# Kernel tuning notes

Hardware: AMD Instinct MI355X
Metric: run time of the kernel (lower is better)

The kernel has to match this reference:

```python
import jax, jax.numpy as jnp
import numpy as np

B, N, DM, H, C, DC = 4, 1024, 512, 8, 3, 16  # batch, nodes, node_dim, heads, manifold components, per-component dim
DK = DM // H


def setup_inputs() -> dict:
    key = jax.random.key(0)
    ks = jax.random.split(key, 8)

    def lin_w(k):
        return jax.random.normal(k, (DM, DM), jnp.float32) / np.sqrt(DM).astype(np.float32)

    return {
        "h": jax.random.normal(ks[0], (B, N, DM), jnp.float32),
        "x": jax.random.normal(ks[1], (B, N, C * DC), jnp.float32),
        "Wq": lin_w(ks[2]), "bq": jnp.zeros((DM,), jnp.float32),
        "Wk": lin_w(ks[3]), "bk": jnp.zeros((DM,), jnp.float32),
        "Wv": lin_w(ks[4]), "bv": jnp.zeros((DM,), jnp.float32),
        "Wo": lin_w(ks[5]), "bo": jnp.zeros((DM,), jnp.float32),
        "alpha": jnp.ones((H, C), jnp.float32),
        "log_sigma": jnp.zeros((H, C), jnp.float32),
    }


def reference(h, x, Wq, bq, Wk, bk, Wv, bv, Wo, bo, alpha, log_sigma):
    b, n, dm = h.shape
    hh, cc = alpha.shape
    dk = dm // hh
    scale = 1.0 / np.sqrt(dk).astype(np.float32)

    def to_heads(t, W, bias):
        return (t @ W.T + bias).reshape(b, n, hh, dk).transpose(0, 2, 1, 3)  # (B,H,N,dk)

    Q = to_heads(h, Wq, bq)
    K = to_heads(h, Wk, bk)
    V = to_heads(h, Wv, bv)

    attn = jnp.einsum('bhid,bhjd->bhij', Q, K) * scale  # (B,H,N,N)

    # Geodesic kernel: per-component Euclidean distances on the product manifold.
    xs = x.reshape(b, n, cc, -1)                      # (B,N,C,dc)
    sq = jnp.sum(xs * xs, axis=-1)                    # (B,N,C)
    inner = jnp.einsum('bicd,bjcd->bijc', xs, xs)     # (B,N,N,C)
    d_sq = jnp.maximum(sq[:, :, None, :] + sq[:, None, :, :] - 2.0 * inner, 0.0)  # (B,N,N,C)

    sigma = jnp.clip(jnp.exp(log_sigma), 1e-4)        # (H,C)
    # exp(-d_c^2 / (2 sigma_{h,c}^2)) -> (B,H,N,N,C), then weight by alpha and sum over c
    e = jnp.exp(-d_sq[:, None] / (2.0 * (sigma ** 2)[None, :, None, None, :])).astype(attn.dtype)
    attn = attn + jnp.einsum('hc,bhijc->bhij', alpha, e)

    p = jax.nn.softmax(attn, axis=-1)
    out = jnp.einsum('bhij,bhjd->bhid', p, V)         # (B,H,N,dk)
    out = out.transpose(0, 2, 1, 3).reshape(b, n, dm)
    return out @ Wo.T + bo
```

## Files before the change

kernel.cpp:

```cpp
#include <hip/hip_runtime.h>
#include <math.h>

typedef __bf16 bf16;
typedef __attribute__((ext_vector_type(8))) __bf16 bf16x8;
typedef __attribute__((ext_vector_type(4))) float f32x4;

#define LOG2E 1.44269504088896f
#define SCALE 0.125f

__device__ inline f32x4 mfma16(bf16x8 a, bf16x8 b, f32x4 c) {
    return __builtin_amdgcn_mfma_f32_16x16x32_bf16(a, b, c, 0, 0, 0);
}
__device__ inline bf16x8 cvt8(float4 v0, float4 v1) {
    bf16x8 o;
    o[0] = (bf16)v0.x; o[1] = (bf16)v0.y; o[2] = (bf16)v0.z; o[3] = (bf16)v0.w;
    o[4] = (bf16)v1.x; o[5] = (bf16)v1.y; o[6] = (bf16)v1.z; o[7] = (bf16)v1.w;
    return o;
}
__device__ inline float fastexp2(float x) {
    float r;
    asm("v_exp_f32 %0, %1" : "=v"(r) : "v"(x));
    return r;
}

__global__ __launch_bounds__(256) void gemm_qkv_kernel(
        const float* __restrict__ A, const float* __restrict__ Wq,
        const float* __restrict__ Wk, const float* __restrict__ Wv,
        const float* __restrict__ bq, const float* __restrict__ bk,
        const float* __restrict__ bv,
        bf16* __restrict__ Qb, bf16* __restrict__ Kb, bf16* __restrict__ Vt) {
    __shared__ bf16 smem[64 * 72 + 128 * 72];
    bf16 (*Asm)[72] = (bf16(*)[72])smem;
    bf16 (*Bsm)[72] = (bf16(*)[72])(smem + 64 * 72);
    int t = threadIdx.x, w = t >> 6, lane = t & 63, g = lane >> 4, lo = lane & 15;
    int rowbase = blockIdx.x * 64, colbase = blockIdx.y * 128;
    int proj = colbase >> 9, wcol = colbase & 511;
    const float* Wsrc = (proj == 0) ? Wq : (proj == 1 ? Wk : Wv);
    const float* bsrc = (proj == 0) ? bq : (proj == 1 ? bk : bv);
    int wr = (w >> 1) * 32, wc = (w & 1) * 64;
    f32x4 acc[2][4] = {};
    int arow = t >> 2, acol = (t & 3) * 16;
    int brow = t >> 1, bcol = (t & 1) * 32;
    for (int kb = 0; kb < 512; kb += 64) {
        __syncthreads();
        {
            const float4* as = (const float4*)&A[(size_t)(rowbase + arow) * 512 + kb + acol];
            *(bf16x8*)&Asm[arow][acol]     = cvt8(as[0], as[1]);
            *(bf16x8*)&Asm[arow][acol + 8] = cvt8(as[2], as[3]);
            const float4* bs = (const float4*)&Wsrc[(size_t)(wcol + brow) * 512 + kb + bcol];
            *(bf16x8*)&Bsm[brow][bcol]      = cvt8(bs[0], bs[1]);
            *(bf16x8*)&Bsm[brow][bcol + 8]  = cvt8(bs[2], bs[3]);
            *(bf16x8*)&Bsm[brow][bcol + 16] = cvt8(bs[4], bs[5]);
            *(bf16x8*)&Bsm[brow][bcol + 24] = cvt8(bs[6], bs[7]);
        }
        __syncthreads();
        for (int kk = 0; kk < 64; kk += 32) {
            bf16x8 af[2], bfr[4];
            for (int m = 0; m < 2; m++) af[m]  = *(const bf16x8*)&Asm[wr + 16 * m + lo][kk + 8 * g];
            for (int n = 0; n < 4; n++) bfr[n] = *(const bf16x8*)&Bsm[wc + 16 * n + lo][kk + 8 * g];
            for (int m = 0; m < 2; m++)
                for (int n = 0; n < 4; n++)
                    acc[m][n] = mfma16(af[m], bfr[n], acc[m][n]);
        }
    }
    __syncthreads();
    bf16 (*Cl)[132] = (bf16(*)[132])smem;
    for (int n = 0; n < 4; n++) {
        float bv = bsrc[wcol + wc + 16 * n + lo];
        for (int m = 0; m < 2; m++)
            for (int r = 0; r < 4; r++)
                Cl[wr + 16 * m + 4 * g + r][wc + 16 * n + lo] = (bf16)(acc[m][n][r] + bv);
    }
    __syncthreads();
    int h0 = (colbase >> 6) & 7;
    int bidx = rowbase >> 10, i0g = rowbase & 1023;
    if (proj < 2) {
        int row = t >> 2, q4 = t & 3;
        int head = h0 + (q4 >> 1), d0 = (q4 & 1) * 32;
        bf16* dst = (proj == 0 ? Qb : Kb) +
                    ((size_t)(bidx * 8 + head) * 1024 + i0g + row) * 64 + d0;
        for (int ch = 0; ch < 4; ch++)
            *(bf16x8*)&dst[ch * 8] = *(const bf16x8*)&Cl[row][(q4 >> 1) * 64 + d0 + ch * 8];
    } else {
        int dcol = t >> 1, ihalf = t & 1;
        int head = h0 + (dcol >> 6), d = dcol & 63;
        bf16* dst = Vt + ((size_t)(bidx * 8 + head) * 64 + d) * 1024 + i0g + ihalf * 32;
        for (int ch = 0; ch < 4; ch++) {
            bf16x8 v;
            for (int q = 0; q < 8; q++) v[q] = Cl[ihalf * 32 + ch * 8 + q][dcol];
            *(bf16x8*)&dst[ch * 8] = v;
        }
    }
}

__global__ __launch_bounds__(256) void attn_kernel(
        const bf16* __restrict__ Qb, const bf16* __restrict__ Kb,
        const bf16* __restrict__ Vt, const float* __restrict__ x,
        const float* __restrict__ alpha, const float* __restrict__ log_sigma,
        float* __restrict__ o_part, float* __restrict__ l_part) {
    __shared__ bf16 Klds[64][72];
    __shared__ bf16 VTlds[64][72];
    __shared__ bf16 Xlds[64][80];
    __shared__ bf16 Plds[4][16][72];

    int t = threadIdx.x;
    int w = t >> 6, lane = t & 63, g = lane >> 4, lo = lane & 15;
    int zz = blockIdx.z;
    int b = zz >> 1, split = zz & 1;
    int hh = blockIdx.y;
    int i0 = blockIdx.x * 64 + w * 16;

    float c1 = SCALE * LOG2E;
    float k2[3], alf[3];
    for (int c = 0; c < 3; c++) {
        float sg = fmaxf(expf(log_sigma[hh * 3 + c]), 1e-4f);
        k2[c] = LOG2E / (sg * sg);
        alf[c] = alpha[hh * 3 + c] * LOG2E;
    }

    const bf16* Qbase = Qb + ((size_t)(b * 8 + hh) * 1024 + i0) * 64;
    bf16x8 qa[2];
    qa[0] = *(const bf16x8*)&Qbase[lo * 64 + 8 * g];
    qa[1] = *(const bf16x8*)&Qbase[lo * 64 + 32 + 8 * g];

    bf16x8 xqa[3];
    for (int c = 0; c < 3; c++) {
        bf16x8 v = {};
        if (g < 2) {
            const float4* xs = (const float4*)&x[((size_t)(b << 10) + i0 + lo) * 48 + c * 16 + 8 * g];
            v = cvt8(xs[0], xs[1]);
        } else if (g == 2) {
            const float* xr = &x[((size_t)(b << 10) + i0 + lo) * 48 + c * 16];
            float s = 0.0f;
            for (int k = 0; k < 16; k++) {
                float vv = (float)(bf16)xr[k];
                s += vv * vv;
            }
            s = -0.5f * s;
            bf16 sh = (bf16)s;
            v[0] = sh;
            v[1] = (bf16)(s - (float)sh);
            v[2] = (bf16)1.0f;
            v[3] = (bf16)1.0f;
        }
        xqa[c] = v;
    }

    bf16x8 ones;
    for (int e = 0; e < 8; e++) ones[e] = (bf16)1.0f;
    f32x4 o[4] = {};
    f32x4 lacc = {};

    for (int idx = t; idx < 64; idx += 256)
        *(uint4*)&Xlds[idx][72] = (uint4){0, 0, 0, 0};

    int sr = t >> 2, sc = (t & 3) * 16;
    int jb = split * 512;
    for (int j0 = jb; j0 < jb + 512; j0 += 64) {
        __syncthreads();
        const bf16* Kbase = Kb + ((size_t)(b * 8 + hh) * 1024 + j0) * 64;
        *(bf16x8*)&Klds[sr][sc]     = *(const bf16x8*)&Kbase[sr * 64 + sc];
        *(bf16x8*)&Klds[sr][sc + 8] = *(const bf16x8*)&Kbase[sr * 64 + sc + 8];
        const bf16* Vbase = Vt + ((size_t)(b * 8 + hh) * 64) * 1024 + j0;
        *(bf16x8*)&VTlds[sr][sc]     = *(const bf16x8*)&Vbase[sr * 1024 + sc];
        *(bf16x8*)&VTlds[sr][sc + 8] = *(const bf16x8*)&Vbase[sr * 1024 + sc + 8];
        if (t < 192) {
            int xr = t / 3, c = t - xr * 3;
            const float4* xs = (const float4*)&x[((size_t)(b << 10) + j0 + xr) * 48 + c * 16];
            bf16x8 d0 = cvt8(xs[0], xs[1]);
            bf16x8 d1 = cvt8(xs[2], xs[3]);
            *(bf16x8*)&Xlds[xr][c * 24]     = d0;
            *(bf16x8*)&Xlds[xr][c * 24 + 8] = d1;
            float s = 0.0f;
            for (int k = 0; k < 8; k++) {
                float a0 = (float)d0[k], a1 = (float)d1[k];
                s += a0 * a0 + a1 * a1;
            }
            s = -0.5f * s;
            bf16 sh = (bf16)s;
            bf16x8 cst = {};
            cst[0] = (bf16)1.0f;
            cst[1] = (bf16)1.0f;
            cst[2] = sh;
            cst[3] = (bf16)(s - (float)sh);
            *(bf16x8*)&Xlds[xr][c * 24 + 16] = cst;
        }
        __syncthreads();

        for (int tt = 0; tt < 4; tt++) {
            f32x4 acc = {};
            bf16x8 kb0 = *(const bf16x8*)&Klds[16 * tt + lo][8 * g];
            bf16x8 kb1 = *(const bf16x8*)&Klds[16 * tt + lo][32 + 8 * g];
            __builtin_amdgcn_s_setprio(1);
            acc = mfma16(qa[0], kb0, acc);
            acc = mfma16(qa[1], kb1, acc);
            f32x4 z0 = {}, z1 = {}, z2 = {};
            f32x4 e0 = mfma16(xqa[0], *(const bf16x8*)&Xlds[16 * tt + lo][8 * g], z0);
            f32x4 e1 = mfma16(xqa[1], *(const bf16x8*)&Xlds[16 * tt + lo][24 + 8 * g], z1);
            f32x4 e2 = mfma16(xqa[2], *(const bf16x8*)&Xlds[16 * tt + lo][48 + 8 * g], z2);
            __builtin_amdgcn_s_setprio(0);
            for (int r = 0; r < 4; r++) {
                float t0 = alf[0] * fastexp2(k2[0] * fminf(e0[r], 0.0f));
                t0 = fmaf(alf[1], fastexp2(k2[1] * fminf(e1[r], 0.0f)), t0);
                t0 = fmaf(alf[2], fastexp2(k2[2] * fminf(e2[r], 0.0f)), t0);
                float p = fastexp2(fmaf(acc[r], c1, t0));
                Plds[w][4 * g + r][16 * tt + lo] = (bf16)p;
            }
        }

        bf16x8 pa0 = *(const bf16x8*)&Plds[w][lo][8 * g];
        bf16x8 pa1 = *(const bf16x8*)&Plds[w][lo][32 + 8 * g];
        __builtin_amdgcn_s_setprio(1);
        lacc = mfma16(pa0, ones, lacc);
        lacc = mfma16(pa1, ones, lacc);
        for (int td = 0; td < 4; td++) {
            bf16x8 vb0 = *(const bf16x8*)&VTlds[16 * td + lo][8 * g];
            bf16x8 vb1 = *(const bf16x8*)&VTlds[16 * td + lo][32 + 8 * g];
            o[td] = mfma16(pa0, vb0, o[td]);
            o[td] = mfma16(pa1, vb1, o[td]);
        }
        __builtin_amdgcn_s_setprio(0);
    }

    for (int td = 0; td < 4; td++)
        for (int r = 0; r < 4; r++) {
            size_t rowg = (size_t)(b * 8 + hh) * 1024 + i0 + 4 * g + r;
            o_part[((size_t)split * 32768 + rowg) * 64 + 16 * td + lo] = o[td][r];
        }
    if (lo == 0)
        for (int r = 0; r < 4; r++) {
            size_t rowg = (size_t)(b * 8 + hh) * 1024 + i0 + 4 * g + r;
            l_part[(size_t)split * 32768 + rowg] = lacc[r];
        }
}

__global__ __launch_bounds__(256) void gemm_out_kernel(
        const float* __restrict__ o_part, const float* __restrict__ l_part,
        const float* __restrict__ Wo, const float* __restrict__ bo,
        float* __restrict__ out) {
    __shared__ bf16 Asm[64][72];
    __shared__ bf16 Bsm[64][72];
    int t = threadIdx.x, w = t >> 6, lane = t & 63, g = lane >> 4, lo = lane & 15;
    int rowbase = blockIdx.x * 64, colbase = blockIdx.y * 64;
    int wr = (w >> 1) * 32, wc = (w & 1) * 32;
    f32x4 acc[2][2] = {};
    int srow = t >> 2, scol = (t & 3) * 16;
    for (int kb = 0; kb < 512; kb += 64) {
        __syncthreads();
        {
            int hh = kb >> 6;
            int n = rowbase + srow;
            size_t rowg = (size_t)((n >> 10) * 8 + hh) * 1024 + (n & 1023);
            const float* p0 = &o_part[rowg * 64 + scol];
            const float* p1 = &o_part[((size_t)32768 + rowg) * 64 + scol];
            float inv = 1.0f / (l_part[rowg] + l_part[32768 + rowg]);
            float4 a0 = ((const float4*)p0)[0], a1 = ((const float4*)p0)[1];
            float4 a2 = ((const float4*)p0)[2], a3 = ((const float4*)p0)[3];
            float4 c0 = ((const float4*)p1)[0], c1 = ((const float4*)p1)[1];
            float4 c2 = ((const float4*)p1)[2], c3 = ((const float4*)p1)[3];
            bf16x8 r0, r1;
            r0[0] = (bf16)((a0.x + c0.x) * inv); r0[1] = (bf16)((a0.y + c0.y) * inv);
            r0[2] = (bf16)((a0.z + c0.z) * inv); r0[3] = (bf16)((a0.w + c0.w) * inv);
            r0[4] = (bf16)((a1.x + c1.x) * inv); r0[5] = (bf16)((a1.y + c1.y) * inv);
            r0[6] = (bf16)((a1.z + c1.z) * inv); r0[7] = (bf16)((a1.w + c1.w) * inv);
            r1[0] = (bf16)((a2.x + c2.x) * inv); r1[1] = (bf16)((a2.y + c2.y) * inv);
            r1[2] = (bf16)((a2.z + c2.z) * inv); r1[3] = (bf16)((a2.w + c2.w) * inv);
            r1[4] = (bf16)((a3.x + c3.x) * inv); r1[5] = (bf16)((a3.y + c3.y) * inv);
            r1[6] = (bf16)((a3.z + c3.z) * inv); r1[7] = (bf16)((a3.w + c3.w) * inv);
            *(bf16x8*)&Asm[srow][scol]     = r0;
            *(bf16x8*)&Asm[srow][scol + 8] = r1;
        }
        {
            const float4* bs = (const float4*)&Wo[(size_t)(colbase + srow) * 512 + kb + scol];
            *(bf16x8*)&Bsm[srow][scol]     = cvt8(bs[0], bs[1]);
            *(bf16x8*)&Bsm[srow][scol + 8] = cvt8(bs[2], bs[3]);
        }
        __syncthreads();
        for (int kk = 0; kk < 64; kk += 32) {
            bf16x8 af[2], bfr[2];
            for (int m = 0; m < 2; m++) af[m]  = *(const bf16x8*)&Asm[wr + 16 * m + lo][kk + 8 * g];
            for (int n = 0; n < 2; n++) bfr[n] = *(const bf16x8*)&Bsm[wc + 16 * n + lo][kk + 8 * g];
            for (int m = 0; m < 2; m++)
                for (int n = 0; n < 2; n++)
                    acc[m][n] = mfma16(af[m], bfr[n], acc[m][n]);
        }
    }
    for (int n = 0; n < 2; n++) {
        int mcol = colbase + wc + 16 * n + lo;
        float bv = bo[mcol];
        for (int m = 0; m < 2; m++)
            for (int r = 0; r < 4; r++)
                out[(size_t)(rowbase + wr + 16 * m + 4 * g + r) * 512 + mcol] =
                    acc[m][n][r] + bv;
    }
}

extern "C" void kernel_launch(void* const* d_in, const int* in_sizes, int n_in,
                              void* d_out, int out_size, void* d_ws, size_t ws_size,
                              hipStream_t stream) {
    const float* h  = (const float*)d_in[0];
    const float* x  = (const float*)d_in[1];
    const float* Wq = (const float*)d_in[2];
    const float* bq = (const float*)d_in[3];
    const float* Wk = (const float*)d_in[4];
    const float* bk = (const float*)d_in[5];
    const float* Wv = (const float*)d_in[6];
    const float* bv = (const float*)d_in[7];
    const float* Wo = (const float*)d_in[8];
    const float* bo = (const float*)d_in[9];
    const float* alpha     = (const float*)d_in[10];
    const float* log_sigma = (const float*)d_in[11];
    float* out = (float*)d_out;

    char* ws = (char*)d_ws;
    size_t off = 0;
    auto alloc = [&](size_t bytes) {
        char* p = ws + off;
        off += (bytes + 255) & ~(size_t)255;
        return p;
    };
    bf16*  Qb     = (bf16*)alloc((size_t)4 * 8 * 1024 * 64 * 2);
    bf16*  Kb     = (bf16*)alloc((size_t)4 * 8 * 1024 * 64 * 2);
    bf16*  Vt     = (bf16*)alloc((size_t)4 * 8 * 1024 * 64 * 2);
    float* o_part = (float*)alloc((size_t)2 * 32768 * 64 * 4);
    float* l_part = (float*)alloc((size_t)2 * 32768 * 4);

    gemm_qkv_kernel<<<dim3(64, 12), 256, 0, stream>>>(h, Wq, Wk, Wv, bq, bk, bv,
                                                      Qb, Kb, Vt);
    attn_kernel<<<dim3(16, 8, 8), 256, 0, stream>>>(
        Qb, Kb, Vt, x, alpha, log_sigma, o_part, l_part);
    gemm_out_kernel<<<dim3(64, 8), 256, 0, stream>>>(o_part, l_part, Wo, bo, out);
}
```

Baseline: 169.5 us.

## Prefetch next tile's global loads into registers across all three kernels

Each main loop in the QKV GEMM, the fused attention kernel and the output GEMM now issues the global loads for the next K-tile into registers right after the LDS barrier, before the MFMA work. The aim is to overlap global memory latency with compute instead of stalling at the top of each iteration. MFMA sections are wrapped in s_setprio, and the output normalisation uses a v_rcp_f32 reciprocal instead of a divide. This raises register pressure, which could lower occupancy.

Measured after the change: 172.6 us. No clear change (+1.8%).

```diff
diff --git a/kernel.cpp b/kernel.cpp
--- a/kernel.cpp
+++ b/kernel.cpp
@@ -20,6 +20,11 @@
 __device__ inline float fastexp2(float x) {
     float r;
     asm("v_exp_f32 %0, %1" : "=v"(r) : "v"(x));
+    return r;
+}
+__device__ inline float fastrcp(float x) {
+    float r;
+    asm("v_rcp_f32 %0, %1" : "=v"(r) : "v"(x));
     return r;
 }
 
@@ -41,19 +46,31 @@
     f32x4 acc[2][4] = {};
     int arow = t >> 2, acol = (t & 3) * 16;
     int brow = t >> 1, bcol = (t & 1) * 32;
+    const float* aptr = &A[(size_t)(rowbase + arow) * 512 + acol];
+    const float* bptr = &Wsrc[(size_t)(wcol + brow) * 512 + bcol];
+    float4 ar[4], br[8];
+    {
+        const float4* as = (const float4*)aptr;
+        ar[0] = as[0]; ar[1] = as[1]; ar[2] = as[2]; ar[3] = as[3];
+        const float4* bs = (const float4*)bptr;
+        for (int q = 0; q < 8; q++) br[q] = bs[q];
+    }
     for (int kb = 0; kb < 512; kb += 64) {
         __syncthreads();
-        {
-            const float4* as = (const float4*)&A[(size_t)(rowbase + arow) * 512 + kb + acol];
-            *(bf16x8*)&Asm[arow][acol]     = cvt8(as[0], as[1]);
-            *(bf16x8*)&Asm[arow][acol + 8] = cvt8(as[2], as[3]);
-            const float4* bs = (const float4*)&Wsrc[(size_t)(wcol + brow) * 512 + kb + bcol];
-            *(bf16x8*)&Bsm[brow][bcol]      = cvt8(bs[0], bs[1]);
-            *(bf16x8*)&Bsm[brow][bcol + 8]  = cvt8(bs[2], bs[3]);
-            *(bf16x8*)&Bsm[brow][bcol + 16] = cvt8(bs[4], bs[5]);
-            *(bf16x8*)&Bsm[brow][bcol + 24] = cvt8(bs[6], bs[7]);
-        }
-        __syncthreads();
+        *(bf16x8*)&Asm[arow][acol]     = cvt8(ar[0], ar[1]);
+        *(bf16x8*)&Asm[arow][acol + 8] = cvt8(ar[2], ar[3]);
+        *(bf16x8*)&Bsm[brow][bcol]      = cvt8(br[0], br[1]);
+        *(bf16x8*)&Bsm[brow][bcol + 8]  = cvt8(br[2], br[3]);
+        *(bf16x8*)&Bsm[brow][bcol + 16] = cvt8(br[4], br[5]);
+        *(bf16x8*)&Bsm[brow][bcol + 24] = cvt8(br[6], br[7]);
+        __syncthreads();
+        if (kb + 64 < 512) {
+            const float4* as = (const float4*)(aptr + kb + 64);
+            ar[0] = as[0]; ar[1] = as[1]; ar[2] = as[2]; ar[3] = as[3];
+            const float4* bs = (const float4*)(bptr + kb + 64);
+            for (int q = 0; q < 8; q++) br[q] = bs[q];
+        }
+        __builtin_amdgcn_s_setprio(1);
         for (int kk = 0; kk < 64; kk += 32) {
             bf16x8 af[2], bfr[4];
             for (int m = 0; m < 2; m++) af[m]  = *(const bf16x8*)&Asm[wr + 16 * m + lo][kk + 8 * g];
@@ -62,6 +79,7 @@
                 for (int n = 0; n < 4; n++)
                     acc[m][n] = mfma16(af[m], bfr[n], acc[m][n]);
         }
+        __builtin_amdgcn_s_setprio(0);
     }
     __syncthreads();
     bf16 (*Cl)[132] = (bf16(*)[132])smem;
@@ -155,22 +173,36 @@
         *(uint4*)&Xlds[idx][72] = (uint4){0, 0, 0, 0};
 
     int sr = t >> 2, sc = (t & 3) * 16;
+    int xr = t / 3, xc = t - xr * 3;
+    const bf16* Kbase0 = Kb + (size_t)(b * 8 + hh) * 1024 * 64;
+    const bf16* Vbase  = Vt + (size_t)(b * 8 + hh) * 64 * 1024;
     int jb = split * 512;
+
+    bf16x8 pk0, pk1, pv0, pv1;
+    float4 pxs[4];
+    {
+        const bf16* Kp = Kbase0 + (size_t)jb * 64;
+        pk0 = *(const bf16x8*)&Kp[sr * 64 + sc];
+        pk1 = *(const bf16x8*)&Kp[sr * 64 + sc + 8];
+        pv0 = *(const bf16x8*)&Vbase[sr * 1024 + jb + sc];
+        pv1 = *(const bf16x8*)&Vbase[sr * 1024 + jb + sc + 8];
+        if (t < 192) {
+            const float4* xs = (const float4*)&x[((size_t)(b << 10) + jb + xr) * 48 + xc * 16];
+            for (int q = 0; q < 4; q++) pxs[q] = xs[q];
+        }
+    }
+
     for (int j0 = jb; j0 < jb + 512; j0 += 64) {
         __syncthreads();
-        const bf16* Kbase = Kb + ((size_t)(b * 8 + hh) * 1024 + j0) * 64;
-        *(bf16x8*)&Klds[sr][sc]     = *(const bf16x8*)&Kbase[sr * 64 + sc];
-        *(bf16x8*)&Klds[sr][sc + 8] = *(const bf16x8*)&Kbase[sr * 64 + sc + 8];
-        const bf16* Vbase = Vt + ((size_t)(b * 8 + hh) * 64) * 1024 + j0;
-        *(bf16x8*)&VTlds[sr][sc]     = *(const bf16x8*)&Vbase[sr * 1024 + sc];
-        *(bf16x8*)&VTlds[sr][sc + 8] = *(const bf16x8*)&Vbase[sr * 1024 + sc + 8];
+        *(bf16x8*)&Klds[sr][sc]      = pk0;
+        *(bf16x8*)&Klds[sr][sc + 8]  = pk1;
+        *(bf16x8*)&VTlds[sr][sc]     = pv0;
+        *(bf16x8*)&VTlds[sr][sc + 8] = pv1;
         if (t < 192) {
-            int xr = t / 3, c = t - xr * 3;
-            const float4* xs = (const float4*)&x[((size_t)(b << 10) + j0 + xr) * 48 + c * 16];
-            bf16x8 d0 = cvt8(xs[0], xs[1]);
-            bf16x8 d1 = cvt8(xs[2], xs[3]);
-            *(bf16x8*)&Xlds[xr][c * 24]     = d0;
-            *(bf16x8*)&Xlds[xr][c * 24 + 8] = d1;
+            bf16x8 d0 = cvt8(pxs[0], pxs[1]);
+            bf16x8 d1 = cvt8(pxs[2], pxs[3]);
+            *(bf16x8*)&Xlds[xr][xc * 24]     = d0;
+            *(bf16x8*)&Xlds[xr][xc * 24 + 8] = d1;
             float s = 0.0f;
             for (int k = 0; k < 8; k++) {
                 float a0 = (float)d0[k], a1 = (float)d1[k];
@@ -183,9 +215,21 @@
             cst[1] = (bf16)1.0f;
             cst[2] = sh;
             cst[3] = (bf16)(s - (float)sh);
-            *(bf16x8*)&Xlds[xr][c * 24 + 16] = cst;
-        }
-        __syncthreads();
+            *(bf16x8*)&Xlds[xr][xc * 24 + 16] = cst;
+        }
+        __syncthreads();
+        if (j0 + 64 < jb + 512) {
+            int jn = j0 + 64;
+            const bf16* Kp = Kbase0 + (size_t)jn * 64;
+            pk0 = *(const bf16x8*)&Kp[sr * 64 + sc];
+            pk1 = *(const bf16x8*)&Kp[sr * 64 + sc + 8];
+            pv0 = *(const bf16x8*)&Vbase[sr * 1024 + jn + sc];
+            pv1 = *(const bf16x8*)&Vbase[sr * 1024 + jn + sc + 8];
+            if (t < 192) {
+                const float4* xs = (const float4*)&x[((size_t)(b << 10) + jn + xr) * 48 + xc * 16];
+                for (int q = 0; q < 4; q++) pxs[q] = xs[q];
+            }
+        }
 
         for (int tt = 0; tt < 4; tt++) {
             f32x4 acc = {};
@@ -245,37 +289,56 @@
     int wr = (w >> 1) * 32, wc = (w & 1) * 32;
     f32x4 acc[2][2] = {};
     int srow = t >> 2, scol = (t & 3) * 16;
+    int n0 = rowbase + srow;
+    size_t rowbase_g = (size_t)((n0 >> 10) * 8) * 1024 + (n0 & 1023);
+
+    float4 pa[4], pc[4], pb[2];
+    float pl0, pl1;
+    {
+        size_t rowg = rowbase_g;
+        const float4* p0 = (const float4*)&o_part[rowg * 64 + scol];
+        const float4* p1 = (const float4*)&o_part[((size_t)32768 + rowg) * 64 + scol];
+        for (int q = 0; q < 4; q++) { pa[q] = p0[q]; pc[q] = p1[q]; }
+        pl0 = l_part[rowg]; pl1 = l_part[32768 + rowg];
+        const float4* bs = (const float4*)&Wo[(size_t)(colbase + srow) * 512 + scol];
+        pb[0] = bs[0]; pb[1] = bs[1];
+    }
+    float4 pb2[2];
+    {
+        const float4* bs = (const float4*)&Wo[(size_t)(colbase + srow) * 512 + scol];
+        pb2[0] = bs[2]; pb2[1] = bs[3];
+    }
+
     for (int kb = 0; kb < 512; kb += 64) {
         __syncthreads();
         {
-            int hh = kb >> 6;
-            int n = rowbase + srow;
-            size_t rowg = (size_t)((n >> 10) * 8 + hh) * 1024 + (n & 1023);
-            const float* p0 = &o_part[rowg * 64 + scol];
-            const float* p1 = &o_part[((size_t)32768 + rowg) * 64 + scol];
-            float inv = 1.0f / (l_part[rowg] + l_part[32768 + rowg]);
-            float4 a0 = ((const float4*)p0)[0], a1 = ((const float4*)p0)[1];
-            float4 a2 = ((const float4*)p0)[2], a3 = ((const float4*)p0)[3];
-            float4 c0 = ((const float4*)p1)[0], c1 = ((const float4*)p1)[1];
-            float4 c2 = ((const float4*)p1)[2], c3 = ((const float4*)p1)[3];
+            float inv = fastrcp(pl0 + pl1);
             bf16x8 r0, r1;
-            r0[0] = (bf16)((a0.x + c0.x) * inv); r0[1] = (bf16)((a0.y + c0.y) * inv);
-            r0[2] = (bf16)((a0.z + c0.z) * inv); r0[3] = (bf16)((a0.w + c0.w) * inv);
-            r0[4] = (bf16)((a1.x + c1.x) * inv); r0[5] = (bf16)((a1.y + c1.y) * inv);
-            r0[6] = (bf16)((a1.z + c1.z) * inv); r0[7] = (bf16)((a1.w + c1.w) * inv);
-            r1[0] = (bf16)((a2.x + c2.x) * inv); r1[1] = (bf16)((a2.y + c2.y) * inv);
-            r1[2] = (bf16)((a2.z + c2.z) * inv); r1[3] = (bf16)((a2.w + c2.w) * inv);
-            r1[4] = (bf16)((a3.x + c3.x) * inv); r1[5] = (bf16)((a3.y + c3.y) * inv);
-            r1[6] = (bf16)((a3.z + c3.z) * inv); r1[7] = (bf16)((a3.w + c3.w) * inv);
+            r0[0] = (bf16)((pa[0].x + pc[0].x) * inv); r0[1] = (bf16)((pa[0].y + pc[0].y) * inv);
+            r0[2] = (bf16)((pa[0].z + pc[0].z) * inv); r0[3] = (bf16)((pa[0].w + pc[0].w) * inv);
+            r0[4] = (bf16)((pa[1].x + pc[1].x) * inv); r0[5] = (bf16)((pa[1].y + pc[1].y) * inv);
+            r0[6] = (bf16)((pa[1].z + pc[1].z) * inv); r0[7] = (bf16)((pa[1].w + pc[1].w) * inv);
+            r1[0] = (bf16)((pa[2].x + pc[2].x) * inv); r1[1] = (bf16)((pa[2].y + pc[2].y) * inv);
+            r1[2] = (bf16)((pa[2].z + pc[2].z) * inv); r1[3] = (bf16)((pa[2].w + pc[2].w) * inv);
+            r1[4] = (bf16)((pa[3].x + pc[3].x) * inv); r1[5] = (bf16)((pa[3].y + pc[3].y) * inv);
+            r1[6] = (bf16)((pa[3].z + pc[3].z) * inv); r1[7] = (bf16)((pa[3].w + pc[3].w) * inv);
             *(bf16x8*)&Asm[srow][scol]     = r0;
             *(bf16x8*)&Asm[srow][scol + 8] = r1;
-        }
-        {
-            const float4* bs = (const float4*)&Wo[(size_t)(colbase + srow) * 512 + kb + scol];
-            *(bf16x8*)&Bsm[srow][scol]     = cvt8(bs[0], bs[1]);
-            *(bf16x8*)&Bsm[srow][scol + 8] = cvt8(bs[2], bs[3]);
-        }
-        __syncthreads();
+            *(bf16x8*)&Bsm[srow][scol]     = cvt8(pb[0], pb[1]);
+            *(bf16x8*)&Bsm[srow][scol + 8] = cvt8(pb2[0], pb2[1]);
+        }
+        __syncthreads();
+        if (kb + 64 < 512) {
+            int hh = (kb >> 6) + 1;
+            size_t rowg = rowbase_g + (size_t)hh * 1024;
+            const float4* p0 = (const float4*)&o_part[rowg * 64 + scol];
+            const float4* p1 = (const float4*)&o_part[((size_t)32768 + rowg) * 64 + scol];
+            for (int q = 0; q < 4; q++) { pa[q] = p0[q]; pc[q] = p1[q]; }
+            pl0 = l_part[rowg]; pl1 = l_part[32768 + rowg];
+            const float4* bs = (const float4*)&Wo[(size_t)(colbase + srow) * 512 + kb + 64 + scol];
+            pb[0] = bs[0]; pb[1] = bs[1]; pb2[0] = bs[2]; pb2[1] = bs[3];
+        }
+        __builtin_amdgcn_s_setprio(1);
         for (int kk = 0; kk < 64; kk += 32) {
             bf16x8 af[2], bfr[2];
             for (int m = 0; m < 2; m++) af[m]  = *(const bf16x8*)&Asm[wr + 16 * m + lo][kk + 8 * g];
@@ -284,6 +347,7 @@
                 for (int n = 0; n < 2; n++)
                     acc[m][n] = mfma16(af[m], bfr[n], acc[m][n]);
         }
+        __builtin_amdgcn_s_setprio(0);
     }
     for (int n = 0; n < 2; n++) {
         int mcol = colbase + wc + 16 * n + lo;
```
